# Kernel optimization log

Measured on AMD Instinct MI355X. Metric: run time of the kernel, lower is better.

## Reference

```python
import jax, jax.numpy as jnp
import numpy as np
import math

N = 100000      # active voxels
K = 27          # 3**3 kernel offsets
L = 50000
INC = 64
OUTC = 64


def setup_inputs() -> dict:
    key = jax.random.key(0)
    k1, k2, k3, k4 = jax.random.split(key, 4)
    features = jax.random.normal(k1, (N, INC), dtype=jnp.float32)
    # kernel init: uniform(-std, std), std = 1/sqrt(inc * k^3)
    std = 1.0 / math.sqrt(INC * K)
    kernel = jax.random.uniform(k2, (K, INC, OUTC), dtype=jnp.float32,
                                minval=-std, maxval=std)
    neighbor_in = jax.random.randint(k3, (K, L), 0, N, dtype=jnp.int32)
    neighbor_out = jax.random.randint(k4, (K, L), 0, N, dtype=jnp.int32)
    return {"features": features, "kernel": kernel,
            "neighbor_in": neighbor_in, "neighbor_out": neighbor_out}


def reference(features, kernel, neighbor_in, neighbor_out):
    # gather -> per-offset GEMM -> scatter-add (torchsparse sparseconv_op, transpose=False)
    gathered = features[neighbor_in]                      # [K, L, INC]
    vals = jnp.einsum('klc,kco->klo', gathered, kernel)    # [K, L, OUTC]
    out = jnp.zeros((features.shape[0], kernel.shape[-1]), dtype=features.dtype)
    out = out.at[neighbor_out.reshape(-1)].add(vals.reshape(-1, kernel.shape[-1]))
    return out
```

## Files before the change

### kernel.cpp

```cpp
#include <hip/hip_runtime.h>
#include <hip/hip_bf16.h>


typedef __bf16 bf16x8 __attribute__((ext_vector_type(8)));
typedef float f32x4 __attribute__((ext_vector_type(4)));

#define KOFF 27
#define SLOTK 4
#define NSLOT (KOFF * SLOTK)
#define OVFCAP 8192
#define WPAD 72
#define ROWCHUNK 8192
#define NIBW (ROWCHUNK / 8)

__global__ __launch_bounds__(256) void kA_rank_cast(
    const float* __restrict__ feat, const float* __restrict__ kern,
    const int* __restrict__ nout, __bf16* __restrict__ fb,
    __bf16* __restrict__ wt, unsigned short* __restrict__ slots,
    int2* __restrict__ ovf, int* __restrict__ ovfcnt, int Lpairs, int nElems,
    int nchunk, int rankBlocks, int wtBlocks) {
  __shared__ unsigned int nib[NIBW];
  if ((int)blockIdx.x < rankBlocks) {
    const int k = blockIdx.x / nchunk;
    const int chunk = blockIdx.x % nchunk;
    const int lo = chunk * ROWCHUNK;
    const int tid = threadIdx.x;
    for (int i = tid; i < NIBW; i += 256) nib[i] = 0u;
    __syncthreads();
    const int* nk = nout + k * Lpairs;
    for (int base = 0; base < Lpairs; base += 2048) {
      int l[8], row[8];
#pragma unroll
      for (int j = 0; j < 8; ++j) {
        l[j] = base + j * 256 + tid;
        row[j] = (l[j] < Lpairs) ? nk[l[j]] : -1;
      }
#pragma unroll
      for (int j = 0; j < 8; ++j) {
        int rr = row[j] - lo;
        if (rr >= 0 && rr < ROWCHUNK) {
          unsigned int sh = ((unsigned)rr & 7u) * 4u;
          unsigned int old = atomicAdd(&nib[rr >> 3], 1u << sh);
          int rank = (old >> sh) & 15;
          if (rank < SLOTK) {
            slots[(size_t)row[j] * NSLOT + k * SLOTK + rank] =
                (unsigned short)l[j];
          } else {
            int idx = atomicAdd(ovfcnt, 1);
            if (idx < OVFCAP) ovf[idx] = make_int2(row[j], k * Lpairs + l[j]);
          }
        }
      }
    }
  } else if ((int)blockIdx.x < rankBlocks + wtBlocks) {
    int kc = (blockIdx.x - rankBlocks) * 256 + threadIdx.x;
    if (kc < KOFF * 64) {
      int k = kc >> 6, c = kc & 63;
      const float* src = kern + k * 4096 + c;
      __bf16* dst = wt + (size_t)kc * 64;
#pragma unroll
      for (int i0 = 0; i0 < 64; i0 += 8) {
        bf16x8 v;
#pragma unroll
        for (int q = 0; q < 8; ++q) v[q] = (__bf16)src[(i0 + q) * 64];
        *(bf16x8*)(dst + i0) = v;
      }
    }
  } else {
    int i = ((blockIdx.x - rankBlocks - wtBlocks) * 256 + threadIdx.x) * 8;
    if (i < nElems) {
      f32x4 a = *(const f32x4*)(feat + i);
      f32x4 b = *(const f32x4*)(feat + i + 4);
      bf16x8 v;
#pragma unroll
      for (int j = 0; j < 4; ++j) {
        v[j] = (__bf16)a[j];
        v[j + 4] = (__bf16)b[j];
      }
      *(bf16x8*)(fb + i) = v;
    }
  }
}

__global__ __launch_bounds__(256) void kF_fused(
    const __bf16* __restrict__ fb, const __bf16* __restrict__ wt,
    const int* __restrict__ nin, const unsigned short* __restrict__ slots,
    float* __restrict__ out, int Lpairs, int Nrows) {
  __shared__ __bf16 ldsW[2][64 * WPAD];
  const int tid = threadIdx.x;
  const int wv = tid >> 6, lane = tid & 63;
  const int r = lane & 15, g = lane >> 4;
  int row = blockIdx.x * 64 + wv * 16 + r;
  if (row >= Nrows) row = Nrows - 1;
  const unsigned short* srow = slots + (size_t)row * NSLOT;

  const int sc = tid >> 2;
  const int si = (tid & 3) * 16;

  {
    const __bf16* wp = wt + sc * 64 + si;
    bf16x8 wa = *(const bf16x8*)(wp);
    bf16x8 wb = *(const bf16x8*)(wp + 8);
    *(bf16x8*)&ldsW[0][sc * WPAD + si] = wa;
    *(bf16x8*)&ldsW[0][sc * WPAD + si + 8] = wb;
  }

  uint2 sv0 = *(const uint2*)(srow);
  uint2 sv1 = *(const uint2*)(srow + SLOTK);
  uint2 sv2 = *(const uint2*)(srow + 2 * SLOTK);
  int e0[4] = {(int)(sv0.x & 0xFFFF), (int)(sv0.x >> 16),
               (int)(sv0.y & 0xFFFF), (int)(sv0.y >> 16)};
  int e1[4] = {(int)(sv1.x & 0xFFFF), (int)(sv1.x >> 16),
               (int)(sv1.y & 0xFFFF), (int)(sv1.y >> 16)};
  int enN[4] = {(int)(sv2.x & 0xFFFF), (int)(sv2.x >> 16),
                (int)(sv2.y & 0xFFFF), (int)(sv2.y >> 16)};
  int gA[4], gB[4], irowNxt[4];
#pragma unroll
  for (int j = 0; j < 4; ++j) gA[j] = (e0[j] != 0xFFFF) ? nin[e0[j]] : -1;
  const int* nin1 = nin + Lpairs;
#pragma unroll
  for (int j = 0; j < 4; ++j) irowNxt[j] = (e1[j] != 0xFFFF) ? nin1[e1[j]] : -1;

  f32x4 acc[4] = {f32x4{0.f, 0.f, 0.f, 0.f}, f32x4{0.f, 0.f, 0.f, 0.f},
                  f32x4{0.f, 0.f, 0.f, 0.f}, f32x4{0.f, 0.f, 0.f, 0.f}};

  __syncthreads();

  bf16x8 faA[4], fcA[4], faB[4], fcB[4];
#pragma unroll
  for (int j = 0; j < 4; ++j) {
    if (gA[j] >= 0) {
      const __bf16* ap = fb + (size_t)gA[j] * 64 + g * 8;
      faA[j] = *(const bf16x8*)(ap);
      fcA[j] = *(const bf16x8*)(ap + 32);
    }
  }

  auto body = [&](int k, bf16x8(&faC)[4], bf16x8(&fcC)[4], int(&gC)[4],
                  bf16x8(&faN)[4], bf16x8(&fcN)[4], int(&gN)[4]) {
    const int kb = k & 1;
    bf16x8 wa, wb;
    if (k + 1 < KOFF) {
      const __bf16* wp = wt + (size_t)(k + 1) * 4096 + sc * 64 + si;
      wa = *(const bf16x8*)(wp);
      wb = *(const bf16x8*)(wp + 8);
    }
#pragma unroll
    for (int j = 0; j < 4; ++j) gN[j] = irowNxt[j];
#pragma unroll
    for (int j = 0; j < 4; ++j) {
      if (gN[j] >= 0) {
        const __bf16* ap = fb + (size_t)gN[j] * 64 + g * 8;
        faN[j] = *(const bf16x8*)(ap);
        fcN[j] = *(const bf16x8*)(ap + 32);
      }
    }
    const int* nin2 = nin + (size_t)(k + 2) * Lpairs;
#pragma unroll
    for (int j = 0; j < 4; ++j)
      irowNxt[j] = (k + 2 < KOFF && enN[j] != 0xFFFF) ? nin2[enN[j]] : -1;
    uint2 sv3 = make_uint2(0xFFFFFFFFu, 0xFFFFFFFFu);
    if (k + 3 < KOFF) sv3 = *(const uint2*)(srow + (k + 3) * SLOTK);
    float s0[8] = {0.f, 0.f, 0.f, 0.f, 0.f, 0.f, 0.f, 0.f};
    float s1[8] = {0.f, 0.f, 0.f, 0.f, 0.f, 0.f, 0.f, 0.f};
#pragma unroll
    for (int j = 0; j < 4; ++j) {
      if (gC[j] >= 0) {
#pragma unroll
        for (int q = 0; q < 8; ++q) {
          s0[q] += (float)faC[j][q];
          s1[q] += (float)fcC[j][q];
        }
      }
    }
    bf16x8 b0, b1;
#pragma unroll
    for (int q = 0; q < 8; ++q) {
      b0[q] = (__bf16)s0[q];
      b1[q] = (__bf16)s1[q];
    }
    bf16x8 w0f[4], w1f[4];
#pragma unroll
    for (int t = 0; t < 4; ++t) {
      w0f[t] = *(const bf16x8*)&ldsW[kb][(t * 16 + r) * WPAD + g * 8];
      w1f[t] = *(const bf16x8*)&ldsW[kb][(t * 16 + r) * WPAD + g * 8 + 32];
    }
#pragma unroll
    for (int t = 0; t < 4; ++t) {
      acc[t] = __builtin_amdgcn_mfma_f32_16x16x32_bf16(w0f[t], b0, acc[t], 0, 0, 0);
      acc[t] = __builtin_amdgcn_mfma_f32_16x16x32_bf16(w1f[t], b1, acc[t], 0, 0, 0);
    }
    if (k + 1 < KOFF) {
      *(bf16x8*)&ldsW[kb ^ 1][sc * WPAD + si] = wa;
      *(bf16x8*)&ldsW[kb ^ 1][sc * WPAD + si + 8] = wb;
      __syncthreads();
    }
    enN[0] = (int)(sv3.x & 0xFFFF);
    enN[1] = (int)(sv3.x >> 16);
    enN[2] = (int)(sv3.y & 0xFFFF);
    enN[3] = (int)(sv3.y >> 16);
  };

  for (int k = 0; k + 1 < KOFF; k += 2) {
    body(k, faA, fcA, gA, faB, fcB, gB);
    body(k + 1, faB, fcB, gB, faA, fcA, gA);
  }
  body(KOFF - 1, faA, fcA, gA, faB, fcB, gB);

  float* op = out + (size_t)row * 64;
#pragma unroll
  for (int t = 0; t < 4; ++t) *(f32x4*)(op + t * 16 + g * 4) = acc[t];
}

__global__ __launch_bounds__(256) void k4_fixup(
    const __bf16* __restrict__ fb, const __bf16* __restrict__ wt,
    const int* __restrict__ nin, const int2* __restrict__ ovf,
    const int* __restrict__ ovfcnt, float* __restrict__ out, int Lpairs) {
  int gid = blockIdx.x * 256 + threadIdx.x;
  int i = gid >> 6, c = gid & 63;
  int n = *ovfcnt;
  if (n > OVFCAP) n = OVFCAP;
  if (i >= n) return;
  int row = ovf[i].x, pid = ovf[i].y;
  int k = pid / Lpairs;
  int irow = nin[pid];
  const __bf16* wk = wt + ((size_t)k * 64 + c) * 64;
  const __bf16* f = fb + (size_t)irow * 64;
  float s = 0.f;
#pragma unroll 8
  for (int q = 0; q < 64; ++q) s += (float)f[q] * (float)wk[q];
  atomicAdd(&out[(size_t)row * 64 + c], s);
}

__global__ __launch_bounds__(256) void spconv_atomic_kernel(
    const float* __restrict__ feat, const float* __restrict__ kern,
    const int* __restrict__ nin, const int* __restrict__ nout,
    float* __restrict__ out, int Lpairs, int blocksPerK) {
  __shared__ __bf16 ldsBT[64 * WPAD];
  const int bk = blockIdx.x / blocksPerK;
  const int chunk = blockIdx.x % blocksPerK;
  const float* kb = kern + bk * 4096;
  for (int idx = threadIdx.x; idx < 4096; idx += 256) {
    int i = idx >> 6, c = idx & 63;
    ldsBT[c * WPAD + i] = (__bf16)kb[idx];
  }
  __syncthreads();
  const int lane = threadIdx.x & 63;
  const int wave = threadIdx.x >> 6;
  const int r = lane & 15, g = lane >> 4;
  bf16x8 bfrag[2][4];
#pragma unroll
  for (int s = 0; s < 2; ++s)
#pragma unroll
    for (int t = 0; t < 4; ++t)
      bfrag[s][t] = *(const bf16x8*)&ldsBT[(t * 16 + r) * WPAD + g * 8 + s * 32];
  const int* ninK = nin + bk * Lpairs;
  const int* noutK = nout + bk * Lpairs;
  const int base0 = chunk * 512 + wave * 128;
  for (int it = 0; it < 8; ++it) {
    const int base = base0 + it * 16;
    if (base >= Lpairs) break;
    const int arow = ninK[base + r];
    const float* ap = feat + (size_t)arow * 64 + g * 8;
    f32x4 f0 = *(const f32x4*)(ap);
    f32x4 f1 = *(const f32x4*)(ap + 4);
    f32x4 f2 = *(const f32x4*)(ap + 32);
    f32x4 f3 = *(const f32x4*)(ap + 36);
    bf16x8 a0, a1;
#pragma unroll
    for (int j = 0; j < 4; ++j) {
      a0[j] = (__bf16)f0[j];
      a0[j + 4] = (__bf16)f1[j];
      a1[j] = (__bf16)f2[j];
      a1[j + 4] = (__bf16)f3[j];
    }
    f32x4 acc[4] = {f32x4{0.f, 0.f, 0.f, 0.f}, f32x4{0.f, 0.f, 0.f, 0.f},
                    f32x4{0.f, 0.f, 0.f, 0.f}, f32x4{0.f, 0.f, 0.f, 0.f}};
#pragma unroll
    for (int t = 0; t < 4; ++t) {
      acc[t] = __builtin_amdgcn_mfma_f32_16x16x32_bf16(a0, bfrag[0][t], acc[t], 0, 0, 0);
      acc[t] = __builtin_amdgcn_mfma_f32_16x16x32_bf16(a1, bfrag[1][t], acc[t], 0, 0, 0);
    }
    int orow[4];
#pragma unroll
    for (int reg = 0; reg < 4; ++reg) orow[reg] = noutK[base + g * 4 + reg];
#pragma unroll
    for (int t = 0; t < 4; ++t)
#pragma unroll
      for (int reg = 0; reg < 4; ++reg)
        atomicAdd(out + (size_t)orow[reg] * 64 + t * 16 + r, acc[t][reg]);
  }
}

extern "C" void kernel_launch(void* const* d_in, const int* in_sizes, int n_in,
                              void* d_out, int out_size, void* d_ws, size_t ws_size,
                              hipStream_t stream) {
  const float* feat = (const float*)d_in[0];
  const float* kern = (const float*)d_in[1];
  const int* nin = (const int*)d_in[2];
  const int* nout = (const int*)d_in[3];
  float* out = (float*)d_out;

  const int total = in_sizes[2];
  const int Lpairs = total / KOFF;
  const int Nrows = out_size / 64;
  const int nElems = Nrows * 64;

  const size_t slotsBytes = (size_t)Nrows * NSLOT * 2;
  const size_t ovfOff = (slotsBytes + 255) & ~(size_t)255;
  const size_t cntOff = (ovfOff + (size_t)OVFCAP * 8 + 255) & ~(size_t)255;
  const size_t wtOff = (cntOff + 256 + 255) & ~(size_t)255;
  const size_t fbOff = (wtOff + (size_t)KOFF * 4096 * 2 + 255) & ~(size_t)255;
  const size_t needed = fbOff + (size_t)nElems * 2;

  const bool shapeOK = (Lpairs <= 65535) && (Lpairs % 16 == 0) &&
                       (total % KOFF == 0) && (out_size % 64 == 0);

  if (shapeOK && ws_size >= needed) {
    unsigned short* slots = (unsigned short*)d_ws;
    int2* ovf = (int2*)((char*)d_ws + ovfOff);
    int* ovfcnt = (int*)((char*)d_ws + cntOff);
    __bf16* wt = (__bf16*)((char*)d_ws + wtOff);
    __bf16* fb = (__bf16*)((char*)d_ws + fbOff);

    hipMemsetAsync(slots, 0xFF, slotsBytes, stream);
    hipMemsetAsync(ovfcnt, 0, 4, stream);

    const int nchunk = (Nrows + ROWCHUNK - 1) / ROWCHUNK;
    const int rankBlocks = KOFF * nchunk;
    const int wtBlocks = (KOFF * 64 + 255) / 256;
    const int castBlocks = (nElems / 8 + 255) / 256;
    kA_rank_cast<<<rankBlocks + wtBlocks + castBlocks, 256, 0, stream>>>(
        feat, kern, nout, fb, wt, slots, ovf, ovfcnt, Lpairs, nElems, nchunk,
        rankBlocks, wtBlocks);
    kF_fused<<<(Nrows + 63) / 64, 256, 0, stream>>>(fb, wt, nin, slots, out,
                                                    Lpairs, Nrows);
    k4_fixup<<<OVFCAP * 64 / 256, 256, 0, stream>>>(fb, wt, nin, ovf, ovfcnt,
                                                    out, Lpairs);
  } else {
    const int blocksPerK = (Lpairs + 511) / 512;
    hipMemsetAsync(d_out, 0, (size_t)out_size * sizeof(float), stream);
    spconv_atomic_kernel<<<KOFF * blocksPerK, 256, 0, stream>>>(
        feat, kern, nin, nout, out, Lpairs, blocksPerK);
  }
}
```

Before: 138.6 us.

## Stage weights in 7-offset LDS chunks with 512-thread blocks, drop feature prefetch

The fused kernel now uses 512-thread blocks covering 128 rows. Instead of double-buffering one weight tile per offset with a barrier every offset, it loads up to 7 offsets' weight tiles into LDS at a time, so there are only four barrier phases. The register-level prefetch of the next offset's gathered features is removed, and features are now loaded in the same iteration they are used. This cuts barrier count and register pressure but raises LDS use to about 63KB per block, which limits occupancy, and it exposes gather latency.

```diff
diff --git a/kernel.cpp b/kernel.cpp
--- a/kernel.cpp
+++ b/kernel.cpp
@@ -10,6 +10,8 @@
 #define NSLOT (KOFF * SLOTK)
 #define OVFCAP 8192
 #define WPAD 72
+#define WTILE (64 * WPAD)
+#define KCH 7
 #define ROWCHUNK 8192
 #define NIBW (ROWCHUNK / 8)
 
@@ -82,28 +84,20 @@
   }
 }
 
-__global__ __launch_bounds__(256) void kF_fused(
+__global__ __launch_bounds__(512) void kF_fused(
     const __bf16* __restrict__ fb, const __bf16* __restrict__ wt,
     const int* __restrict__ nin, const unsigned short* __restrict__ slots,
     float* __restrict__ out, int Lpairs, int Nrows) {
-  __shared__ __bf16 ldsW[2][64 * WPAD];
+  __shared__ __bf16 ldsW[KCH * WTILE];
   const int tid = threadIdx.x;
   const int wv = tid >> 6, lane = tid & 63;
   const int r = lane & 15, g = lane >> 4;
-  int row = blockIdx.x * 64 + wv * 16 + r;
+  int row = blockIdx.x * 128 + wv * 16 + r;
   if (row >= Nrows) row = Nrows - 1;
   const unsigned short* srow = slots + (size_t)row * NSLOT;
 
-  const int sc = tid >> 2;
-  const int si = (tid & 3) * 16;
-
-  {
-    const __bf16* wp = wt + sc * 64 + si;
-    bf16x8 wa = *(const bf16x8*)(wp);
-    bf16x8 wb = *(const bf16x8*)(wp + 8);
-    *(bf16x8*)&ldsW[0][sc * WPAD + si] = wa;
-    *(bf16x8*)&ldsW[0][sc * WPAD + si + 8] = wb;
-  }
+  const int sc = tid >> 3;
+  const int si = (tid & 7) * 8;
 
   uint2 sv0 = *(const uint2*)(srow);
   uint2 sv1 = *(const uint2*)(srow + SLOTK);
@@ -114,9 +108,9 @@
                (int)(sv1.y & 0xFFFF), (int)(sv1.y >> 16)};
   int enN[4] = {(int)(sv2.x & 0xFFFF), (int)(sv2.x >> 16),
                 (int)(sv2.y & 0xFFFF), (int)(sv2.y >> 16)};
-  int gA[4], gB[4], irowNxt[4];
-#pragma unroll
-  for (int j = 0; j < 4; ++j) gA[j] = (e0[j] != 0xFFFF) ? nin[e0[j]] : -1;
+  int irowCur[4], irowNxt[4];
+#pragma unroll
+  for (int j = 0; j < 4; ++j) irowCur[j] = (e0[j] != 0xFFFF) ? nin[e0[j]] : -1;
   const int* nin1 = nin + Lpairs;
 #pragma unroll
   for (int j = 0; j < 4; ++j) irowNxt[j] = (e1[j] != 0xFFFF) ? nin1[e1[j]] : -1;
@@ -124,52 +118,32 @@
   f32x4 acc[4] = {f32x4{0.f, 0.f, 0.f, 0.f}, f32x4{0.f, 0.f, 0.f, 0.f},
                   f32x4{0.f, 0.f, 0.f, 0.f}, f32x4{0.f, 0.f, 0.f, 0.f}};
 
-  __syncthreads();
-
-  bf16x8 faA[4], fcA[4], faB[4], fcB[4];
-#pragma unroll
-  for (int j = 0; j < 4; ++j) {
-    if (gA[j] >= 0) {
-      const __bf16* ap = fb + (size_t)gA[j] * 64 + g * 8;
-      faA[j] = *(const bf16x8*)(ap);
-      fcA[j] = *(const bf16x8*)(ap + 32);
-    }
-  }
-
-  auto body = [&](int k, bf16x8(&faC)[4], bf16x8(&fcC)[4], int(&gC)[4],
-                  bf16x8(&faN)[4], bf16x8(&fcN)[4], int(&gN)[4]) {
-    const int kb = k & 1;
-    bf16x8 wa, wb;
-    if (k + 1 < KOFF) {
-      const __bf16* wp = wt + (size_t)(k + 1) * 4096 + sc * 64 + si;
-      wa = *(const bf16x8*)(wp);
-      wb = *(const bf16x8*)(wp + 8);
-    }
-#pragma unroll
-    for (int j = 0; j < 4; ++j) gN[j] = irowNxt[j];
+  auto body = [&](int k, int kk) {
+    bf16x8 fa[4], fc[4];
 #pragma unroll
     for (int j = 0; j < 4; ++j) {
-      if (gN[j] >= 0) {
-        const __bf16* ap = fb + (size_t)gN[j] * 64 + g * 8;
-        faN[j] = *(const bf16x8*)(ap);
-        fcN[j] = *(const bf16x8*)(ap + 32);
+      if (irowCur[j] >= 0) {
+        const __bf16* ap = fb + (size_t)irowCur[j] * 64 + g * 8;
+        fa[j] = *(const bf16x8*)(ap);
+        fc[j] = *(const bf16x8*)(ap + 32);
       }
     }
     const int* nin2 = nin + (size_t)(k + 2) * Lpairs;
+    int irowN2[4];
 #pragma unroll
     for (int j = 0; j < 4; ++j)
-      irowNxt[j] = (k + 2 < KOFF && enN[j] != 0xFFFF) ? nin2[enN[j]] : -1;
+      irowN2[j] = (k + 2 < KOFF && enN[j] != 0xFFFF) ? nin2[enN[j]] : -1;
     uint2 sv3 = make_uint2(0xFFFFFFFFu, 0xFFFFFFFFu);
     if (k + 3 < KOFF) sv3 = *(const uint2*)(srow + (k + 3) * SLOTK);
     float s0[8] = {0.f, 0.f, 0.f, 0.f, 0.f, 0.f, 0.f, 0.f};
     float s1[8] = {0.f, 0.f, 0.f, 0.f, 0.f, 0.f, 0.f, 0.f};
 #pragma unroll
     for (int j = 0; j < 4; ++j) {
-      if (gC[j] >= 0) {
+      if (irowCur[j] >= 0) {
 #pragma unroll
         for (int q = 0; q < 8; ++q) {
-          s0[q] += (float)faC[j][q];
-          s1[q] += (float)fcC[j][q];
+          s0[q] += (float)fa[j][q];
+          s1[q] += (float)fc[j][q];
         }
       }
     }
@@ -182,18 +156,18 @@
     bf16x8 w0f[4], w1f[4];
 #pragma unroll
     for (int t = 0; t < 4; ++t) {
-      w0f[t] = *(const bf16x8*)&ldsW[kb][(t * 16 + r) * WPAD + g * 8];
-      w1f[t] = *(const bf16x8*)&ldsW[kb][(t * 16 + r) * WPAD + g * 8 + 32];
+      w0f[t] = *(const bf16x8*)&ldsW[kk * WTILE + (t * 16 + r) * WPAD + g * 8];
+      w1f[t] = *(const bf16x8*)&ldsW[kk * WTILE + (t * 16 + r) * WPAD + g * 8 + 32];
     }
 #pragma unroll
     for (int t = 0; t < 4; ++t) {
       acc[t] = __builtin_amdgcn_mfma_f32_16x16x32_bf16(w0f[t], b0, acc[t], 0, 0, 0);
       acc[t] = __builtin_amdgcn_mfma_f32_16x16x32_bf16(w1f[t], b1, acc[t], 0, 0, 0);
     }
-    if (k + 1 < KOFF) {
-      *(bf16x8*)&ldsW[kb ^ 1][sc * WPAD + si] = wa;
-      *(bf16x8*)&ldsW[kb ^ 1][sc * WPAD + si + 8] = wb;
-      __syncthreads();
+#pragma unroll
+    for (int j = 0; j < 4; ++j) {
+      irowCur[j] = irowNxt[j];
+      irowNxt[j] = irowN2[j];
     }
     enN[0] = (int)(sv3.x & 0xFFFF);
     enN[1] = (int)(sv3.x >> 16);
@@ -201,11 +175,22 @@
     enN[3] = (int)(sv3.y >> 16);
   };
 
-  for (int k = 0; k + 1 < KOFF; k += 2) {
-    body(k, faA, fcA, gA, faB, fcB, gB);
-    body(k + 1, faB, fcB, gB, faA, fcA, gA);
-  }
-  body(KOFF - 1, faA, fcA, gA, faB, fcB, gB);
+  int kbase = 0;
+#pragma unroll 1
+  for (int c = 0; c < 4; ++c) {
+    const int kcnt = (c < 3) ? KCH : (KOFF - 3 * KCH);
+    if (c) __syncthreads();
+#pragma unroll
+    for (int kk = 0; kk < KCH; ++kk) {
+      if (kk < kcnt) {
+        bf16x8 w = *(const bf16x8*)(wt + (size_t)(kbase + kk) * 4096 + sc * 64 + si);
+        *(bf16x8*)&ldsW[kk * WTILE + sc * WPAD + si] = w;
+      }
+    }
+    __syncthreads();
+    for (int kk = 0; kk < kcnt; ++kk) body(kbase + kk, kk);
+    kbase += kcnt;
+  }
 
   float* op = out + (size_t)row * 64;
 #pragma unroll
@@ -333,8 +318,8 @@
     kA_rank_cast<<<rankBlocks + wtBlocks + castBlocks, 256, 0, stream>>>(
         feat, kern, nout, fb, wt, slots, ovf, ovfcnt, Lpairs, nElems, nchunk,
         rankBlocks, wtBlocks);
-    kF_fused<<<(Nrows + 63) / 64, 256, 0, stream>>>(fb, wt, nin, slots, out,
-                                                    Lpairs, Nrows);
+    kF_fused<<<(Nrows + 127) / 128, 512, 0, stream>>>(fb, wt, nin, slots, out,
+                                                      Lpairs, Nrows);
     k4_fixup<<<OVFCAP * 64 / 256, 256, 0, stream>>>(fb, wt, nin, ovf, ovfcnt,
                                                     out, Lpairs);
   } else {
```

Result: no change. 138.5 us (-0.1%).
